# Performance work log

Hardware: AMD Instinct MI355X
Metric: run time of the kernel (lower is better)

The kernel has to match this reference:

```python
import jax, jax.numpy as jnp
import numpy as np

N = 100000
E = 1600000
F_IN = 128
HID = 128
CLS = 40
K = 3  # TAGConv default hops for both layers


def setup_inputs() -> dict:
    key = jax.random.key(0)
    k_x, k_e, k_w1, k_b1, k_w2, k_b2 = jax.random.split(key, 6)
    x = jax.random.normal(k_x, (N, F_IN), dtype=jnp.float32)
    edge_index = jax.random.randint(k_e, (2, E), 0, N, dtype=jnp.int64)
    # TAGConv params: K+1 linear maps (no per-lin bias) + one output bias
    s1 = 1.0 / np.sqrt(F_IN)
    s2 = 1.0 / np.sqrt(HID)
    w1 = jax.random.uniform(k_w1, (K + 1, F_IN, HID), jnp.float32, -s1, s1)
    b1 = jnp.zeros((HID,), jnp.float32)
    w2 = jax.random.uniform(k_w2, (K + 1, HID, CLS), jnp.float32, -s2, s2)
    b2 = jnp.zeros((CLS,), jnp.float32)
    return {"x": x, "edge_index": edge_index, "w1": w1, "b1": b1, "w2": w2, "b2": b2}


def _gcn_norm(edge_index, num_nodes):
    # gcn_norm with add_self_loops=False (TAGConv behavior), edge_weight = 1
    row, col = edge_index[0], edge_index[1]
    deg = jax.ops.segment_sum(jnp.ones((edge_index.shape[1],), jnp.float32), col,
                              num_segments=num_nodes)
    dis = jnp.where(deg > 0, jax.lax.rsqrt(jnp.maximum(deg, 1.0)), 0.0)
    return dis[row] * dis[col]


def _tagconv(x, ws, b, row, col, norm):
    # out = sum_k ( (D^-1/2 A D^-1/2)^k x ) @ W_k + b
    out = x @ ws[0]
    h = x
    for k in range(1, ws.shape[0]):
        # SpMM: h_new[col] += norm * h[row]
        h = jax.ops.segment_sum(h[row] * norm[:, None], col, num_segments=x.shape[0])
        out = out + h @ ws[k]
    return out + b


def reference(x, edge_index, w1, b1, w2, b2):
    row, col = edge_index[0], edge_index[1]
    norm = _gcn_norm(edge_index, x.shape[0])
    h = jax.nn.relu(_tagconv(x, w1, b1, row, col, norm))
    # dropout: module in eval mode -> identity
    out = _tagconv(h, w2, b2, row, col, norm)
    return jax.nn.log_softmax(out, axis=1)
```

## Files before the change

### kernel.cpp

```cpp
#include <hip/hip_runtime.h>
#include <math.h>

typedef __bf16 bf16x8 __attribute__((ext_vector_type(8)));
typedef float  f32x4  __attribute__((ext_vector_type(4)));
typedef unsigned u32x4 __attribute__((ext_vector_type(4)));

__device__ __forceinline__ unsigned short f2bf(float f){
  unsigned u = __float_as_uint(f);
  unsigned r = (u + 0x7fffu + ((u>>16)&1u)) >> 16;
  return (unsigned short)r;
}
__device__ __forceinline__ float bflo(unsigned v){ return __uint_as_float(v<<16); }
__device__ __forceinline__ float bfhi(unsigned v){ return __uint_as_float(v & 0xffff0000u); }


#define PT 4096

__global__ void __launch_bounds__(256) k_phist(const int* __restrict__ colv,
                                               int* __restrict__ hcnt, int E){
  __shared__ int lh[512];
  int tid = threadIdx.x;
  for(int i=tid;i<512;i+=256) lh[i]=0;
  __syncthreads();
  int base = blockIdx.x*PT;
  int bmax = E - base; if(bmax > PT) bmax = PT;
  for(int k=tid;k<bmax;k+=256){
    int c = colv[base+k];
    atomicAdd(&lh[c>>8],1);
  }
  __syncthreads();
  for(int i=tid;i<512;i+=256){
    int cnt = lh[i];
    if(cnt>0) atomicAdd(&hcnt[i],cnt);
  }
}

__global__ void __launch_bounds__(512) k_bscan(const int* __restrict__ hcnt,
                                               int* __restrict__ bbase, int* __restrict__ gcur,
                                               int* __restrict__ rowptr, int NB, int N){
  __shared__ int ts[512];
  int tid = threadIdx.x;
  int v = (tid<NB) ? hcnt[tid] : 0;
  ts[tid]=v; __syncthreads();
  for(int o=1;o<512;o<<=1){
    int t=(tid>=o)?ts[tid-o]:0; __syncthreads();
    ts[tid]+=t; __syncthreads();
  }
  int ex = ts[tid]-v;
  if(tid<=NB) bbase[tid] = (tid<NB) ? ex : ts[NB-1];
  if(tid<NB)  gcur[tid]  = ex;
  if(tid==0)  rowptr[N]  = ts[511];
}


__global__ void __launch_bounds__(256) k_part(const int* __restrict__ rowv,
                                              const int* __restrict__ colv,
                                              int* __restrict__ gcur,
                                              unsigned* __restrict__ part, int E){
  __shared__ int lh[512];
  __shared__ int lb[512];
  int tid = threadIdx.x;
  for(int i=tid;i<512;i+=256) lh[i]=0;
  __syncthreads();
  int base = blockIdx.x*PT;
  int bmax = E - base; if(bmax > PT) bmax = PT;
  for(int k=tid;k<bmax;k+=256){
    int c = colv[base+k];
    atomicAdd(&lh[c>>8],1);
  }
  __syncthreads();
  for(int i=tid;i<512;i+=256){
    int cnt = lh[i];
    lb[i] = cnt>0 ? atomicAdd(&gcur[i],cnt) : 0;
  }
  __syncthreads();
  for(int i=tid;i<512;i+=256) lh[i]=0;
  __syncthreads();
  for(int k=tid;k<bmax;k+=256){
    int r = rowv[base+k], c = colv[base+k];
    int b = c>>8;
    int pos = lb[b] + atomicAdd(&lh[b],1);
    part[pos] = ((unsigned)(c&255)<<24) | (unsigned)r;
  }
}


#define CAP 6144

__global__ void __launch_bounds__(256) k_csort(const unsigned* __restrict__ part,
                                               const int* __restrict__ bbase,
                                               float* __restrict__ dis,
                                               unsigned* __restrict__ ed4,
                                               int* __restrict__ rowptr, int N){
  __shared__ unsigned st[CAP];
  __shared__ int cnt[256];
  __shared__ int ts[256];
  int b = blockIdx.x, tid = threadIdx.x;
  int nb0 = b<<8;
  int g0 = bbase[b], g1 = bbase[b+1];
  int ce = g1-g0;
  cnt[tid]=0; __syncthreads();
  for(int i=tid;i<ce;i+=256){
    atomicAdd(&cnt[part[g0+i]>>24],1);
  }
  __syncthreads();
  int v = cnt[tid];
  ts[tid]=v; __syncthreads();
  for(int o=1;o<256;o<<=1){
    int t=(tid>=o)?ts[tid-o]:0; __syncthreads();
    ts[tid]+=t; __syncthreads();
  }
  int ex = ts[tid]-v;
  int node = nb0+tid;
  if(node < N){
    rowptr[node] = g0 + ex;
    dis[node] = v > 0 ? rsqrtf((float)v) : 0.f;
  }
  cnt[tid] = ex;
  __syncthreads();
  for(int i=tid;i<ce;i+=256){
    unsigned pc = part[g0+i];
    int pos = atomicAdd(&cnt[pc>>24],1);
    if(pos < CAP) st[pos] = pc & 0xFFFFFFu;
  }
  __syncthreads();
  for(int i=tid;i<ce;i+=256) ed4[g0+i] = st[i];
}


__global__ void __launch_bounds__(256) k_wfill(const unsigned* __restrict__ ed4,
                                               const int* __restrict__ rowptr,
                                               const float* __restrict__ dis,
                                               uint2* __restrict__ ed8, int N){
  int wid = threadIdx.x>>6, lane = threadIdx.x&63;
  int n = blockIdx.x*4 + wid;
  if(n>=N) return;
  int s = rowptr[n], e = rowptr[n+1];
  float dc = dis[n];
  for(int i=s+lane; i<e; i+=64){
    unsigned r = ed4[i];
    ed8[i] = make_uint2(r, __float_as_uint(dis[r]*dc));
  }
}


__global__ void k_cast_x(const float* __restrict__ x, ushort* __restrict__ xb, int n4){
  int t = blockIdx.x*256 + threadIdx.x;
  if(t < n4){
    float4 v = ((const float4*)x)[t];
    uint2 o;
    o.x = (unsigned)f2bf(v.x) | ((unsigned)f2bf(v.y)<<16);
    o.y = (unsigned)f2bf(v.z) | ((unsigned)f2bf(v.w)<<16);
    ((uint2*)xb)[t] = o;
  }
}

__global__ void k_castw1(const float* __restrict__ w1, ushort* __restrict__ w1t){
  int i = blockIdx.x*256 + threadIdx.x;
  int n = i & 127, kin = (i>>7)&127, s = i>>14;
  w1t[n*512 + s*128 + kin] = f2bf(w1[i]);
}

__global__ void k_castw2(const float* __restrict__ w2, ushort* __restrict__ w2t){
  int i = blockIdx.x*256 + threadIdx.x;
  int k = i & 127, np = i>>7;
  int s = np>>6, nn = np&63;
  float v = (nn<40) ? w2[(s*128 + k)*40 + nn] : 0.f;
  w2t[i] = f2bf(v);
}


#define FMA8(vv, ww) \
  a[0]+=ww*bflo(vv.x); a[1]+=ww*bfhi(vv.x); \
  a[2]+=ww*bflo(vv.y); a[3]+=ww*bfhi(vv.y); \
  a[4]+=ww*bflo(vv.z); a[5]+=ww*bfhi(vv.z); \
  a[6]+=ww*bflo(vv.w); a[7]+=ww*bfhi(vv.w);

__global__ void __launch_bounds__(256) k_spmm1(
    const ushort* __restrict__ src, ushort* __restrict__ dst,
    const int* __restrict__ rowptr, const uint2* __restrict__ ed, int N){
  int tid = threadIdx.x;
  int lane = tid & 63;
  int gl = tid & 15;
  int gbase = lane & 48;
  int n = blockIdx.x*16 + (tid>>4);
  if(n>=N) return;
  int s = rowptr[n], e = rowptr[n+1];
  float a[8];
  #pragma unroll
  for(int i=0;i<8;i++) a[i]=0.f;
  for(int b=s; b<e; b+=16){
    uint2 eD = make_uint2(0u,0u);
    if(b+gl < e) eD = ed[b+gl];
    #pragma unroll
    for(int t=0;t<4;t++){
      int j = gbase + 4*t;
      int r0 = __shfl((int)eD.x, j);
      int r1 = __shfl((int)eD.x, j+1);
      int r2 = __shfl((int)eD.x, j+2);
      int r3 = __shfl((int)eD.x, j+3);
      float w0 = __uint_as_float(__shfl((int)eD.y, j));
      float w1 = __uint_as_float(__shfl((int)eD.y, j+1));
      float w2 = __uint_as_float(__shfl((int)eD.y, j+2));
      float w3 = __uint_as_float(__shfl((int)eD.y, j+3));
      uint4 v0 = *(const uint4*)(src + (size_t)r0*128 + gl*8);
      uint4 v1 = *(const uint4*)(src + (size_t)r1*128 + gl*8);
      uint4 v2 = *(const uint4*)(src + (size_t)r2*128 + gl*8);
      uint4 v3 = *(const uint4*)(src + (size_t)r3*128 + gl*8);
      FMA8(v0, w0)
      FMA8(v1, w1)
      FMA8(v2, w2)
      FMA8(v3, w3)
    }
  }
  u32x4 o;
  o.x = (unsigned)f2bf(a[0]) | ((unsigned)f2bf(a[1])<<16);
  o.y = (unsigned)f2bf(a[2]) | ((unsigned)f2bf(a[3])<<16);
  o.z = (unsigned)f2bf(a[4]) | ((unsigned)f2bf(a[5])<<16);
  o.w = (unsigned)f2bf(a[6]) | ((unsigned)f2bf(a[7])<<16);
  __builtin_nontemporal_store(o, (u32x4*)(dst + (size_t)n*128 + gl*8));
}


__global__ void __launch_bounds__(256) k_spmm2(
    const ushort* __restrict__ tprev, int ss,
    const ushort* __restrict__ z, int zs,
    ushort* __restrict__ tnew,
    const int* __restrict__ rowptr, const uint2* __restrict__ ed, int N){
  int tid = threadIdx.x;
  int lane = tid & 63;
  int gl = tid & 7;
  int gbase = lane & 56;
  int n = blockIdx.x*32 + (tid>>3);
  if(n>=N) return;
  int s = rowptr[n], e = rowptr[n+1];
  float a[8];
  #pragma unroll
  for(int i=0;i<8;i++) a[i]=0.f;
  for(int b=s; b<e; b+=8){
    uint2 eD = make_uint2(0u,0u);
    if(b+gl < e) eD = ed[b+gl];
    #pragma unroll
    for(int t=0;t<2;t++){
      int j = gbase + 4*t;
      int r0 = __shfl((int)eD.x, j);
      int r1 = __shfl((int)eD.x, j+1);
      int r2 = __shfl((int)eD.x, j+2);
      int r3 = __shfl((int)eD.x, j+3);
      float w0 = __uint_as_float(__shfl((int)eD.y, j));
      float w1 = __uint_as_float(__shfl((int)eD.y, j+1));
      float w2 = __uint_as_float(__shfl((int)eD.y, j+2));
      float w3 = __uint_as_float(__shfl((int)eD.y, j+3));
      uint4 v0 = *(const uint4*)(tprev + (size_t)r0*ss + gl*8);
      uint4 v1 = *(const uint4*)(tprev + (size_t)r1*ss + gl*8);
      uint4 v2 = *(const uint4*)(tprev + (size_t)r2*ss + gl*8);
      uint4 v3 = *(const uint4*)(tprev + (size_t)r3*ss + gl*8);
      FMA8(v0, w0)
      FMA8(v1, w1)
      FMA8(v2, w2)
      FMA8(v3, w3)
    }
  }
  uint4 vz = *(const uint4*)(z + (size_t)n*zs + gl*8);
  a[0]+=bflo(vz.x); a[1]+=bfhi(vz.x);
  a[2]+=bflo(vz.y); a[3]+=bfhi(vz.y);
  a[4]+=bflo(vz.z); a[5]+=bfhi(vz.z);
  a[6]+=bflo(vz.w); a[7]+=bfhi(vz.w);
  u32x4 o;
  o.x = (unsigned)f2bf(a[0]) | ((unsigned)f2bf(a[1])<<16);
  o.y = (unsigned)f2bf(a[2]) | ((unsigned)f2bf(a[3])<<16);
  o.z = (unsigned)f2bf(a[4]) | ((unsigned)f2bf(a[5])<<16);
  o.w = (unsigned)f2bf(a[6]) | ((unsigned)f2bf(a[7])<<16);
  __builtin_nontemporal_store(o, (u32x4*)(tnew + (size_t)n*64 + gl*8));
}


__global__ void __launch_bounds__(256) k_spmm2_lsm(
    const ushort* __restrict__ tprev, int ss,
    const ushort* __restrict__ z, int zs,
    float* __restrict__ out,
    const int* __restrict__ rowptr, const uint2* __restrict__ ed, int N){
  int tid = threadIdx.x;
  int lane = tid & 63;
  int gl = tid & 7;
  int gbase = lane & 56;
  int n = blockIdx.x*32 + (tid>>3);
  if(n>=N) return;
  int s = rowptr[n], e = rowptr[n+1];
  float a[8];
  #pragma unroll
  for(int i=0;i<8;i++) a[i]=0.f;
  for(int b=s; b<e; b+=8){
    uint2 eD = make_uint2(0u,0u);
    if(b+gl < e) eD = ed[b+gl];
    #pragma unroll
    for(int t=0;t<2;t++){
      int j = gbase + 4*t;
      int r0 = __shfl((int)eD.x, j);
      int r1 = __shfl((int)eD.x, j+1);
      int r2 = __shfl((int)eD.x, j+2);
      int r3 = __shfl((int)eD.x, j+3);
      float w0 = __uint_as_float(__shfl((int)eD.y, j));
      float w1 = __uint_as_float(__shfl((int)eD.y, j+1));
      float w2 = __uint_as_float(__shfl((int)eD.y, j+2));
      float w3 = __uint_as_float(__shfl((int)eD.y, j+3));
      uint4 v0 = *(const uint4*)(tprev + (size_t)r0*ss + gl*8);
      uint4 v1 = *(const uint4*)(tprev + (size_t)r1*ss + gl*8);
      uint4 v2 = *(const uint4*)(tprev + (size_t)r2*ss + gl*8);
      uint4 v3 = *(const uint4*)(tprev + (size_t)r3*ss + gl*8);
      FMA8(v0, w0)
      FMA8(v1, w1)
      FMA8(v2, w2)
      FMA8(v3, w3)
    }
  }
  uint4 vz = *(const uint4*)(z + (size_t)n*zs + gl*8);
  a[0]+=bflo(vz.x); a[1]+=bfhi(vz.x);
  a[2]+=bflo(vz.y); a[3]+=bfhi(vz.y);
  a[4]+=bflo(vz.z); a[5]+=bfhi(vz.z);
  a[6]+=bflo(vz.w); a[7]+=bfhi(vz.w);
  bool valid = (gl < 5);
  float mx = -1e30f;
  #pragma unroll
  for(int i=0;i<8;i++) if(valid) mx = fmaxf(mx, a[i]);
  #pragma unroll
  for(int o=1;o<8;o<<=1) mx = fmaxf(mx, __shfl_xor(mx, o));
  float sum = 0.f;
  #pragma unroll
  for(int i=0;i<8;i++) if(valid) sum += __expf(a[i]-mx);
  #pragma unroll
  for(int o=1;o<8;o<<=1) sum += __shfl_xor(sum, o);
  float l = mx + __logf(sum);
  if(valid){
    f32x4 o0, o1;
    o0[0]=a[0]-l; o0[1]=a[1]-l; o0[2]=a[2]-l; o0[3]=a[3]-l;
    o1[0]=a[4]-l; o1[1]=a[5]-l; o1[2]=a[6]-l; o1[3]=a[7]-l;
    float* op = out + (size_t)n*40 + gl*8;
    __builtin_nontemporal_store(o0, (f32x4*)op);
    __builtin_nontemporal_store(o1, (f32x4*)(op+4));
  }
}


#define LDA 72

__global__ void __launch_bounds__(256) k_gemm1(
    const ushort* __restrict__ xb, const ushort* __restrict__ h1,
    const ushort* __restrict__ h2, const ushort* __restrict__ h3,
    const ushort* __restrict__ w1t, const float* __restrict__ bias,
    ushort* __restrict__ outb, int N){
  __shared__ ushort Al[128*LDA];
  __shared__ ushort Bl[128*LDA];
  int tid = threadIdx.x;
  int wid = tid>>6, lane = tid&63;
  int wr = wid>>1, wc = wid&1;
  int lm = lane&15, kg = lane>>4;
  int nbase = blockIdx.x*128;
  f32x4 acc[4][4];
  #pragma unroll
  for(int i=0;i<4;i++)
    #pragma unroll
    for(int j=0;j<4;j++) acc[i][j] = (f32x4){0.f,0.f,0.f,0.f};

  for(int kc=0; kc<8; kc++){
    const ushort* asrc = (kc<2) ? xb : (kc<4) ? h1 : (kc<6) ? h2 : h3;
    int koff = (kc&1)*64;
    __syncthreads();
    #pragma unroll
    for(int i=0;i<4;i++){
      int slot = tid + i*256;
      int r = slot>>3, seg = (slot&7)*8;
      int n = nbase + r;
      uint4 v = make_uint4(0,0,0,0);
      if(n < N) v = *(const uint4*)(asrc + (size_t)n*128 + koff + seg);
      *(uint4*)(&Al[r*LDA + seg]) = v;
    }
    #pragma unroll
    for(int i=0;i<4;i++){
      int slot = tid + i*256;
      int r = slot>>3, seg = (slot&7)*8;
      uint4 v = *(const uint4*)(w1t + (size_t)r*512 + kc*64 + seg);
      *(uint4*)(&Bl[r*LDA + seg]) = v;
    }
    __syncthreads();
    #pragma unroll
    for(int ks=0; ks<2; ks++){
      bf16x8 a[4], b[4];
      #pragma unroll
      for(int f=0; f<4; f++){
        a[f] = *(const bf16x8*)&Al[(wr*64 + f*16 + lm)*LDA + ks*32 + kg*8];
        b[f] = *(const bf16x8*)&Bl[(wc*64 + f*16 + lm)*LDA + ks*32 + kg*8];
      }
      #pragma unroll
      for(int fm=0; fm<4; fm++)
        #pragma unroll
        for(int fn=0; fn<4; fn++)
          acc[fm][fn] = __builtin_amdgcn_mfma_f32_16x16x32_bf16(a[fm], b[fn], acc[fm][fn], 0,0,0);
    }
  }
  int crow0 = (lane>>4)*4;
  #pragma unroll
  for(int fm=0; fm<4; fm++){
    #pragma unroll
    for(int fn=0; fn<4; fn++){
      int col = wc*64 + fn*16 + lm;
      float bv = bias[col];
      #pragma unroll
      for(int j=0;j<4;j++){
        int row = nbase + wr*64 + fm*16 + crow0 + j;
        if(row < N){
          float v = fmaxf(acc[fm][fn][j] + bv, 0.f);
          outb[(size_t)row*128 + col] = f2bf(v);
        }
      }
    }
  }
}


__global__ void __launch_bounds__(256) k_gemm2(
    const ushort* __restrict__ ab, const ushort* __restrict__ w2t,
    const float* __restrict__ bias, ushort* __restrict__ z, int N){
  __shared__ ushort Al[128*LDA];
  __shared__ ushort Bl[128*LDA];
  int tid = threadIdx.x;
  int wid = tid>>6, lane = tid&63;
  int wr = wid>>1, wc = wid&1;
  int lm = lane&15, kg = lane>>4;
  int nbase = blockIdx.x*128;
  int cb = blockIdx.y;
  f32x4 acc[4][4];
  #pragma unroll
  for(int i=0;i<4;i++)
    #pragma unroll
    for(int j=0;j<4;j++) acc[i][j] = (f32x4){0.f,0.f,0.f,0.f};

  for(int kc=0; kc<2; kc++){
    int koff = kc*64;
    __syncthreads();
    #pragma unroll
    for(int i=0;i<4;i++){
      int slot = tid + i*256;
      int r = slot>>3, seg = (slot&7)*8;
      int n = nbase + r;
      uint4 v = make_uint4(0,0,0,0);
      if(n < N) v = *(const uint4*)(ab + (size_t)n*128 + koff + seg);
      *(uint4*)(&Al[r*LDA + seg]) = v;
    }
    #pragma unroll
    for(int i=0;i<4;i++){
      int slot = tid + i*256;
      int r = slot>>3, seg = (slot&7)*8;
      uint4 v = *(const uint4*)(w2t + (size_t)(cb*128 + r)*128 + koff + seg);
      *(uint4*)(&Bl[r*LDA + seg]) = v;
    }
    __syncthreads();
    #pragma unroll
    for(int ks=0; ks<2; ks++){
      bf16x8 a[4], b[4];
      #pragma unroll
      for(int f=0; f<4; f++){
        a[f] = *(const bf16x8*)&Al[(wr*64 + f*16 + lm)*LDA + ks*32 + kg*8];
        b[f] = *(const bf16x8*)&Bl[(wc*64 + f*16 + lm)*LDA + ks*32 + kg*8];
      }
      #pragma unroll
      for(int fm=0; fm<4; fm++)
        #pragma unroll
        for(int fn=0; fn<4; fn++)
          acc[fm][fn] = __builtin_amdgcn_mfma_f32_16x16x32_bf16(a[fm], b[fn], acc[fm][fn], 0,0,0);
    }
  }
  int crow0 = (lane>>4)*4;
  #pragma unroll
  for(int fm=0; fm<4; fm++){
    #pragma unroll
    for(int fn=0; fn<4; fn++){
      int cc = cb*128 + wc*64 + fn*16 + lm;
      float bv = (cc < 40) ? bias[cc] : 0.f;
      #pragma unroll
      for(int j=0;j<4;j++){
        int row = nbase + wr*64 + fm*16 + crow0 + j;
        if(row < N){
          float v = acc[fm][fn][j] + bv;
          z[(size_t)row*256 + cc] = f2bf(v);
        }
      }
    }
  }
}


extern "C" void kernel_launch(void* const* d_in, const int* in_sizes, int n_in,
                              void* d_out, int out_size, void* d_ws, size_t ws_size,
                              hipStream_t stream){
  const float* x  = (const float*)d_in[0];
  const int*   ei = (const int*)d_in[1];
  const float* w1 = (const float*)d_in[2];
  const float* b1 = (const float*)d_in[3];
  const float* w2 = (const float*)d_in[4];
  const float* b2 = (const float*)d_in[5];
  float* out = (float*)d_out;
  int N = in_sizes[0] / 128;
  int E = in_sizes[1] / 2;
  const int* rowv = ei;
  const int* colv = ei + E;
  int NB = (N + 255) >> 8;

  char* wsp = (char*)d_ws;
  size_t off = 0;
  auto alloc = [&](size_t bytes)->void*{
    void* p = wsp + off;
    off = (off + bytes + 255) & ~(size_t)255;
    return p;
  };
  float*    dis    = (float*)   alloc((size_t)N*4);
  int*      rowptr = (int*)     alloc((size_t)(N+1)*4);
  int*      hcnt   = (int*)     alloc(512*4);
  int*      bbase  = (int*)     alloc(513*4);
  int*      gcur   = (int*)     alloc(512*4);
  unsigned* part   = (unsigned*)alloc((size_t)E*4);
  unsigned* ed4    = (unsigned*)alloc((size_t)E*4);
  uint2*    ed8    = (uint2*)   alloc((size_t)E*8);
  ushort*   xb     = (ushort*)  alloc((size_t)N*128*2);
  ushort*   hb1    = (ushort*)  alloc((size_t)N*128*2);
  ushort*   hb2    = (ushort*)  alloc((size_t)N*128*2);
  ushort*   hb3    = (ushort*)  alloc((size_t)N*128*2);
  ushort*   out1b  = (ushort*)  alloc((size_t)N*128*2);
  ushort*   w1t    = (ushort*)  alloc(128*512*2);
  ushort*   w2t    = (ushort*)  alloc(256*128*2);
  ushort*   zst    = (ushort*)  alloc((size_t)N*256*2);
  ushort*   ta     = hb1;
  ushort*   tb     = hb2;
  (void)ws_size;

  int pb = (E+PT-1)/PT;
  int sg  = (N+3)/4;
  int sg1 = (N+15)/16;
  int sg2 = (N+31)/32;
  int gb  = (N+127)/128;

  hipMemsetAsync(hcnt, 0, 512*4, stream);
  k_phist <<<pb, 256, 0, stream>>>(colv, hcnt, E);
  k_bscan <<<1, 512, 0, stream>>>(hcnt, bbase, gcur, rowptr, NB, N);
  k_part  <<<pb, 256, 0, stream>>>(rowv, colv, gcur, part, E);
  k_csort <<<NB, 256, 0, stream>>>(part, bbase, dis, ed4, rowptr, N);
  k_wfill <<<sg, 256, 0, stream>>>(ed4, rowptr, dis, ed8, N);

  k_cast_x <<<(N*32+255)/256, 256, 0, stream>>>(x, xb, N*32);
  k_castw1 <<<256, 256, 0, stream>>>(w1, w1t);
  k_castw2 <<<128, 256, 0, stream>>>(w2, w2t);

  k_spmm1<<<sg1, 256, 0, stream>>>(xb,  hb1, rowptr, ed8, N);
  k_spmm1<<<sg1, 256, 0, stream>>>(hb1, hb2, rowptr, ed8, N);
  k_spmm1<<<sg1, 256, 0, stream>>>(hb2, hb3, rowptr, ed8, N);
  k_gemm1<<<gb, 256, 0, stream>>>(xb, hb1, hb2, hb3, w1t, b1, out1b, N);
  k_gemm2<<<dim3(gb,2), 256, 0, stream>>>(out1b, w2t, b2, zst, N);
  k_spmm2    <<<sg2, 256, 0, stream>>>(zst+192, 256, zst+128, 256, ta, rowptr, ed8, N);
  k_spmm2    <<<sg2, 256, 0, stream>>>(ta,       64, zst+64,  256, tb, rowptr, ed8, N);
  k_spmm2_lsm<<<sg2, 256, 0, stream>>>(tb,       64, zst,     256, out, rowptr, ed8, N);
}
```

Measured before the change: 467.8 us.

## Use direct global-to-LDS loads with XOR swizzle in GEMMs, fuse cast kernels

```diff
diff --git a/kernel.cpp b/kernel.cpp
--- a/kernel.cpp
+++ b/kernel.cpp
@@ -13,8 +13,13 @@
 __device__ __forceinline__ float bflo(unsigned v){ return __uint_as_float(v<<16); }
 __device__ __forceinline__ float bfhi(unsigned v){ return __uint_as_float(v & 0xffff0000u); }
 
-
-#define PT 4096
+__device__ __forceinline__ void gl_lds16(const void* g, void* l){
+  __builtin_amdgcn_global_load_lds((const __attribute__((address_space(1))) void*)g,
+                                   (__attribute__((address_space(3))) void*)l, 16, 0, 0);
+}
+
+
+#define PT 8192
 
 __global__ void __launch_bounds__(256) k_phist(const int* __restrict__ colv,
                                                int* __restrict__ hcnt, int E){
@@ -144,7 +149,9 @@
 }
 
 
-__global__ void k_cast_x(const float* __restrict__ x, ushort* __restrict__ xb, int n4){
+__global__ void k_cast_all(const float* __restrict__ x, const float* __restrict__ w1,
+                           const float* __restrict__ w2, ushort* __restrict__ xb,
+                           ushort* __restrict__ w1t, ushort* __restrict__ w2t, int n4){
   int t = blockIdx.x*256 + threadIdx.x;
   if(t < n4){
     float4 v = ((const float4*)x)[t];
@@ -153,20 +160,16 @@
     o.y = (unsigned)f2bf(v.z) | ((unsigned)f2bf(v.w)<<16);
     ((uint2*)xb)[t] = o;
   }
-}
-
-__global__ void k_castw1(const float* __restrict__ w1, ushort* __restrict__ w1t){
-  int i = blockIdx.x*256 + threadIdx.x;
-  int n = i & 127, kin = (i>>7)&127, s = i>>14;
-  w1t[n*512 + s*128 + kin] = f2bf(w1[i]);
-}
-
-__global__ void k_castw2(const float* __restrict__ w2, ushort* __restrict__ w2t){
-  int i = blockIdx.x*256 + threadIdx.x;
-  int k = i & 127, np = i>>7;
-  int s = np>>6, nn = np&63;
-  float v = (nn<40) ? w2[(s*128 + k)*40 + nn] : 0.f;
-  w2t[i] = f2bf(v);
+  if(t < 65536){
+    int n = t & 127, kin = (t>>7)&127, s = t>>14;
+    w1t[n*512 + s*128 + kin] = f2bf(w1[t]);
+  }
+  if(t < 32768){
+    int k = t & 127, np = t>>7;
+    int s = np>>6, nn = np&63;
+    float v = (nn<40) ? w2[(s*128 + k)*40 + nn] : 0.f;
+    w2t[t] = f2bf(v);
+  }
 }
 
 
@@ -342,20 +345,19 @@
 }
 
 
-#define LDA 72
-
 __global__ void __launch_bounds__(256) k_gemm1(
     const ushort* __restrict__ xb, const ushort* __restrict__ h1,
     const ushort* __restrict__ h2, const ushort* __restrict__ h3,
     const ushort* __restrict__ w1t, const float* __restrict__ bias,
     ushort* __restrict__ outb, int N){
-  __shared__ ushort Al[128*LDA];
-  __shared__ ushort Bl[128*LDA];
-  int tid = threadIdx.x;
-  int wid = tid>>6, lane = tid&63;
-  int wr = wid>>1, wc = wid&1;
+  __shared__ ushort Al[128*64];
+  __shared__ ushort Bl[128*64];
+  int tid = threadIdx.x;
+  int w = tid>>6, lane = tid&63;
+  int wr = w>>1, wc = w&1;
   int lm = lane&15, kg = lane>>4;
   int nbase = blockIdx.x*128;
+  bool full = (nbase + 128 <= N);
   f32x4 acc[4][4];
   #pragma unroll
   for(int i=0;i<4;i++)
@@ -366,21 +368,40 @@
     const ushort* asrc = (kc<2) ? xb : (kc<4) ? h1 : (kc<6) ? h2 : h3;
     int koff = (kc&1)*64;
     __syncthreads();
-    #pragma unroll
-    for(int i=0;i<4;i++){
-      int slot = tid + i*256;
-      int r = slot>>3, seg = (slot&7)*8;
-      int n = nbase + r;
-      uint4 v = make_uint4(0,0,0,0);
-      if(n < N) v = *(const uint4*)(asrc + (size_t)n*128 + koff + seg);
-      *(uint4*)(&Al[r*LDA + seg]) = v;
-    }
-    #pragma unroll
-    for(int i=0;i<4;i++){
-      int slot = tid + i*256;
-      int r = slot>>3, seg = (slot&7)*8;
-      uint4 v = *(const uint4*)(w1t + (size_t)r*512 + kc*64 + seg);
-      *(uint4*)(&Bl[r*LDA + seg]) = v;
+    if(full){
+      #pragma unroll
+      for(int i=0;i<4;i++){
+        int o = ((i*4 + w)*64 + lane)*16;
+        int r = o>>7, b = o&127;
+        int sb = b ^ ((r&7)<<4);
+        gl_lds16((const char*)asrc + (size_t)(nbase + r)*256 + koff*2 + sb,
+                 (char*)Al + (i*4 + w)*1024);
+      }
+      #pragma unroll
+      for(int i=0;i<4;i++){
+        int o = ((i*4 + w)*64 + lane)*16;
+        int r = o>>7, b = o&127;
+        int sb = b ^ ((r&7)<<4);
+        gl_lds16((const char*)w1t + (size_t)r*1024 + kc*128 + sb,
+                 (char*)Bl + (i*4 + w)*1024);
+      }
+    } else {
+      #pragma unroll
+      for(int i=0;i<4;i++){
+        int slot = tid + i*256;
+        int r = slot>>3, b = (slot&7)*16;
+        int n = nbase + r;
+        uint4 v = make_uint4(0,0,0,0);
+        if(n < N) v = *(const uint4*)((const char*)asrc + (size_t)n*256 + koff*2 + b);
+        *(uint4*)((char*)Al + r*128 + (b ^ ((r&7)<<4))) = v;
+      }
+      #pragma unroll
+      for(int i=0;i<4;i++){
+        int slot = tid + i*256;
+        int r = slot>>3, b = (slot&7)*16;
+        uint4 v = *(const uint4*)((const char*)w1t + (size_t)r*1024 + kc*128 + b);
+        *(uint4*)((char*)Bl + r*128 + (b ^ ((r&7)<<4))) = v;
+      }
     }
     __syncthreads();
     #pragma unroll
@@ -388,8 +409,11 @@
       bf16x8 a[4], b[4];
       #pragma unroll
       for(int f=0; f<4; f++){
-        a[f] = *(const bf16x8*)&Al[(wr*64 + f*16 + lm)*LDA + ks*32 + kg*8];
-        b[f] = *(const bf16x8*)&Bl[(wc*64 + f*16 + lm)*LDA + ks*32 + kg*8];
+        int ra = wr*64 + f*16 + lm;
+        int rb = wc*64 + f*16 + lm;
+        int cb = ks*64 + kg*16;
+        a[f] = *(const bf16x8*)((const char*)Al + ra*128 + (cb ^ ((ra&7)<<4)));
+        b[f] = *(const bf16x8*)((const char*)Bl + rb*128 + (cb ^ ((rb&7)<<4)));
       }
       #pragma unroll
       for(int fm=0; fm<4; fm++)
@@ -421,14 +445,15 @@
 __global__ void __launch_bounds__(256) k_gemm2(
     const ushort* __restrict__ ab, const ushort* __restrict__ w2t,
     const float* __restrict__ bias, ushort* __restrict__ z, int N){
-  __shared__ ushort Al[128*LDA];
-  __shared__ ushort Bl[128*LDA];
-  int tid = threadIdx.x;
-  int wid = tid>>6, lane = tid&63;
-  int wr = wid>>1, wc = wid&1;
+  __shared__ ushort Al[128*64];
+  __shared__ ushort Bl[128*64];
+  int tid = threadIdx.x;
+  int w = tid>>6, lane = tid&63;
+  int wr = w>>1, wc = w&1;
   int lm = lane&15, kg = lane>>4;
   int nbase = blockIdx.x*128;
-  int cb = blockIdx.y;
+  int cb2 = blockIdx.y;
+  bool full = (nbase + 128 <= N);
   f32x4 acc[4][4];
   #pragma unroll
   for(int i=0;i<4;i++)
@@ -438,21 +463,40 @@
   for(int kc=0; kc<2; kc++){
     int koff = kc*64;
     __syncthreads();
-    #pragma unroll
-    for(int i=0;i<4;i++){
-      int slot = tid + i*256;
-      int r = slot>>3, seg = (slot&7)*8;
-      int n = nbase + r;
-      uint4 v = make_uint4(0,0,0,0);
-      if(n < N) v = *(const uint4*)(ab + (size_t)n*128 + koff + seg);
-      *(uint4*)(&Al[r*LDA + seg]) = v;
-    }
-    #pragma unroll
-    for(int i=0;i<4;i++){
-      int slot = tid + i*256;
-      int r = slot>>3, seg = (slot&7)*8;
-      uint4 v = *(const uint4*)(w2t + (size_t)(cb*128 + r)*128 + koff + seg);
-      *(uint4*)(&Bl[r*LDA + seg]) = v;
+    if(full){
+      #pragma unroll
+      for(int i=0;i<4;i++){
+        int o = ((i*4 + w)*64 + lane)*16;
+        int r = o>>7, b = o&127;
+        int sb = b ^ ((r&7)<<4);
+        gl_lds16((const char*)ab + (size_t)(nbase + r)*256 + koff*2 + sb,
+                 (char*)Al + (i*4 + w)*1024);
+      }
+      #pragma unroll
+      for(int i=0;i<4;i++){
+        int o = ((i*4 + w)*64 + lane)*16;
+        int r = o>>7, b = o&127;
+        int sb = b ^ ((r&7)<<4);
+        gl_lds16((const char*)w2t + (size_t)(cb2*128 + r)*256 + koff*2 + sb,
+                 (char*)Bl + (i*4 + w)*1024);
+      }
+    } else {
+      #pragma unroll
+      for(int i=0;i<4;i++){
+        int slot = tid + i*256;
+        int r = slot>>3, b = (slot&7)*16;
+        int n = nbase + r;
+        uint4 v = make_uint4(0,0,0,0);
+        if(n < N) v = *(const uint4*)((const char*)ab + (size_t)n*256 + koff*2 + b);
+        *(uint4*)((char*)Al + r*128 + (b ^ ((r&7)<<4))) = v;
+      }
+      #pragma unroll
+      for(int i=0;i<4;i++){
+        int slot = tid + i*256;
+        int r = slot>>3, b = (slot&7)*16;
+        uint4 v = *(const uint4*)((const char*)w2t + (size_t)(cb2*128 + r)*256 + koff*2 + b);
+        *(uint4*)((char*)Bl + r*128 + (b ^ ((r&7)<<4))) = v;
+      }
     }
     __syncthreads();
     #pragma unroll
@@ -460,8 +504,11 @@
       bf16x8 a[4], b[4];
       #pragma unroll
       for(int f=0; f<4; f++){
-        a[f] = *(const bf16x8*)&Al[(wr*64 + f*16 + lm)*LDA + ks*32 + kg*8];
-        b[f] = *(const bf16x8*)&Bl[(wc*64 + f*16 + lm)*LDA + ks*32 + kg*8];
+        int ra = wr*64 + f*16 + lm;
+        int rb = wc*64 + f*16 + lm;
+        int cbyte = ks*64 + kg*16;
+        a[f] = *(const bf16x8*)((const char*)Al + ra*128 + (cbyte ^ ((ra&7)<<4)));
+        b[f] = *(const bf16x8*)((const char*)Bl + rb*128 + (cbyte ^ ((rb&7)<<4)));
       }
       #pragma unroll
       for(int fm=0; fm<4; fm++)
@@ -475,7 +522,7 @@
   for(int fm=0; fm<4; fm++){
     #pragma unroll
     for(int fn=0; fn<4; fn++){
-      int cc = cb*128 + wc*64 + fn*16 + lm;
+      int cc = cb2*128 + wc*64 + fn*16 + lm;
       float bv = (cc < 40) ? bias[cc] : 0.f;
       #pragma unroll
       for(int j=0;j<4;j++){
@@ -546,9 +593,7 @@
   k_csort <<<NB, 256, 0, stream>>>(part, bbase, dis, ed4, rowptr, N);
   k_wfill <<<sg, 256, 0, stream>>>(ed4, rowptr, dis, ed8, N);
 
-  k_cast_x <<<(N*32+255)/256, 256, 0, stream>>>(x, xb, N*32);
-  k_castw1 <<<256, 256, 0, stream>>>(w1, w1t);
-  k_castw2 <<<128, 256, 0, stream>>>(w2, w2t);
+  k_cast_all<<<(N*32+255)/256, 256, 0, stream>>>(x, w1, w2, xb, w1t, w2t, N*32);
 
   k_spmm1<<<sg1, 256, 0, stream>>>(xb,  hb1, rowptr, ed8, N);
   k_spmm1<<<sg1, 256, 0, stream>>>(hb1, hb2, rowptr, ed8, N);
```

After: 441.9 us (median of 2 runs). -5.5%, faster.
